# Performance work log

Measured on AMD Instinct MI355X. Metric: run time of the kernel, lower is better.

## Reference

```python
import jax, jax.numpy as jnp
import numpy as np

B, S, D, H, F, E, K = 2, 2048, 1024, 16, 4096, 8, 2
DH = D // H
EPS = 1e-6  # RMSNorm eps (torch nn.RMSNorm default ~ fp32 machine eps; 1e-6 used here)


def _rmsnorm(x, w):
    return x * jax.lax.rsqrt(jnp.mean(x * x, axis=-1, keepdims=True) + EPS) * w


def setup_inputs() -> dict:
    key = jax.random.key(0)
    ks = jax.random.split(key, 16)
    std = 0.02
    return {
        "x": jax.random.normal(ks[0], (B, S, D), jnp.float32),
        "norm1_w": jnp.ones((D,), jnp.float32),
        "norm2_w": jnp.ones((D,), jnp.float32),
        "w_qkv": jax.random.normal(ks[1], (D, 3 * D), jnp.float32) * std,
        "b_qkv": jnp.zeros((3 * D,), jnp.float32),
        "w_o": jax.random.normal(ks[2], (D, D), jnp.float32) * std,
        "b_o": jnp.zeros((D,), jnp.float32),
        "router_w": jax.random.normal(ks[3], (D, E), jnp.float32) * std,
        "router_b": jnp.zeros((E,), jnp.float32),
        "w1": jax.random.normal(ks[4], (E, D, F), jnp.float32) * std,
        "b1": jnp.zeros((E, F), jnp.float32),
        "w2": jax.random.normal(ks[5], (E, F, D), jnp.float32) * std,
        "b2": jnp.zeros((E, D), jnp.float32),
    }


def reference(x, norm1_w, norm2_w, w_qkv, b_qkv, w_o, b_o,
              router_w, router_b, w1, b1, w2, b2):
    # ---- pre-norm causal multi-head attention ----
    h = _rmsnorm(x, norm1_w)
    qkv = h @ w_qkv + b_qkv                                  # [B,S,3D]
    q, k, v = jnp.split(qkv, 3, axis=-1)
    q = q.reshape(B, S, H, DH).transpose(0, 2, 1, 3)         # [B,H,S,DH]
    k = k.reshape(B, S, H, DH).transpose(0, 2, 1, 3)
    v = v.reshape(B, S, H, DH).transpose(0, 2, 1, 3)
    scores = jnp.einsum('bhqd,bhkd->bhqk', q, k) / jnp.sqrt(jnp.asarray(DH, x.dtype))
    causal = jnp.tril(jnp.ones((S, S), bool))
    scores = jnp.where(causal, scores, jnp.asarray(-1e9, x.dtype))
    attn = jax.nn.softmax(scores, axis=-1)
    ao = jnp.einsum('bhqk,bhkd->bhqd', attn, v).transpose(0, 2, 1, 3).reshape(B, S, D)
    x = x + (ao @ w_o + b_o)

    # ---- pre-norm top-k MoE feed-forward ----
    h2 = _rmsnorm(x, norm2_w)
    t = h2.reshape(-1, D)                                    # [T,D], T=B*S
    logits = t @ router_w + router_b                         # [T,E]
    probs = jax.nn.softmax(logits, axis=-1)
    topv, topi = jax.lax.top_k(probs, K)                     # [T,K]
    gates_k = topv / jnp.sum(topv, axis=-1, keepdims=True)   # renormalized top-k gates
    oh = jax.nn.one_hot(topi, E, dtype=x.dtype)              # [T,K,E]
    gates = jnp.einsum('tke,tk->te', oh, gates_k)            # dense gates, zero off top-k

    out = jnp.zeros_like(t)
    for e in range(E):                                       # fixed small expert loop
        he = jax.nn.gelu(t @ w1[e] + b1[e], approximate=False)
        ye = he @ w2[e] + b2[e]
        out = out + gates[:, e:e + 1] * ye

    # load-balancing aux loss: E * sum_e f_e * P_e
    f = jnp.mean(jnp.sum(oh, axis=1), axis=0)                # fraction routed to each expert
    P = jnp.mean(probs, axis=0)                              # mean router prob per expert
    aux_loss = jnp.asarray(E, x.dtype) * jnp.sum(f * P)

    x = x + out.reshape(B, S, D)
    return (x, aux_loss)
```

## Files before the change

### kernel.cpp

```cpp
#include <hip/hip_runtime.h>
#include <math.h>

#define TB 2
#define TS 2048
#define TD 1024
#define TH 16
#define TDH 64
#define TF 4096
#define TE 8
#define TT 4096
#define PSTR (TB*TH*TS*TDH)

typedef __attribute__((ext_vector_type(8))) __bf16 bf16x8;
typedef __attribute__((ext_vector_type(4))) float f32x4;
typedef __attribute__((ext_vector_type(8))) short short8;
typedef __attribute__((ext_vector_type(4))) unsigned short ushort4v;
typedef __attribute__((ext_vector_type(4))) float fvec4;

__device__ inline unsigned short f2bf(float f) {
  union { float f; unsigned int u; } v; v.f = f;
  unsigned int u = v.u;
  unsigned int r = (u + 0x7FFFu + ((u >> 16) & 1u)) >> 16;
  return (unsigned short)r;
}
__device__ inline float bf2f(unsigned short h) {
  union { unsigned int u; float f; } v; v.u = ((unsigned int)h) << 16; return v.f;
}
__device__ inline void split2(float x, unsigned short& h, unsigned short& m) {
  h = f2bf(x);
  m = f2bf(x - bf2f(h));
}

__device__ inline f32x4 mfma_bf16(short8 a, short8 b, f32x4 c) {
  return __builtin_amdgcn_mfma_f32_16x16x32_bf16(
      __builtin_bit_cast(bf16x8, a), __builtin_bit_cast(bf16x8, b), c, 0, 0, 0);
}

__device__ inline void gload16(void* g, void* l) {
  __builtin_amdgcn_global_load_lds(
      (__attribute__((address_space(1))) void*)g,
      (__attribute__((address_space(3))) void*)l, 16, 0, 0);
}

__global__ __launch_bounds__(256)
void tcvt_kernel(const float* __restrict__ In, unsigned short* __restrict__ Out,
                 int R, int C) {
  __shared__ float tile[32][33];
  In  += (size_t)blockIdx.z * R * C;
  Out += (size_t)blockIdx.z * R * C;
  int c0 = blockIdx.x * 32, r0 = blockIdx.y * 32;
  int tx = threadIdx.x & 31, ty = threadIdx.x >> 5;
#pragma unroll
  for (int i = 0; i < 4; ++i)
    tile[ty + 8*i][tx] = In[(size_t)(r0 + ty + 8*i) * C + c0 + tx];
  __syncthreads();
#pragma unroll
  for (int i = 0; i < 4; ++i)
    Out[(size_t)(c0 + ty + 8*i) * R + r0 + tx] = f2bf(tile[tx][ty + 8*i]);
}

__global__ __launch_bounds__(256)
void tcvt_split_kernel(const float* __restrict__ In,
                       unsigned short* __restrict__ O0,
                       unsigned short* __restrict__ O1, int R, int C) {
  __shared__ float tile[32][33];
  int c0 = blockIdx.x * 32, r0 = blockIdx.y * 32;
  int tx = threadIdx.x & 31, ty = threadIdx.x >> 5;
#pragma unroll
  for (int i = 0; i < 4; ++i)
    tile[ty + 8*i][tx] = In[(size_t)(r0 + ty + 8*i) * C + c0 + tx];
  __syncthreads();
#pragma unroll
  for (int i = 0; i < 4; ++i) {
    float v = tile[tx][ty + 8*i];
    unsigned short h, m; split2(v, h, m);
    size_t idx = (size_t)(c0 + ty + 8*i) * R + r0 + tx;
    O0[idx] = h; O1[idx] = m;
  }
}

__global__ __launch_bounds__(256)
void rmsnorm_kernel(const float* __restrict__ X, const float* __restrict__ W,
                    unsigned short* __restrict__ O) {
  int row = blockIdx.x;
  int tid = threadIdx.x;
  int lane = tid & 63, wave = tid >> 6;
  const float* xr = X + (size_t)row * TD;
  fvec4 v = *(const fvec4*)(xr + tid * 4);
  float ss = v[0]*v[0] + v[1]*v[1] + v[2]*v[2] + v[3]*v[3];
#pragma unroll
  for (int msk = 1; msk < 64; msk <<= 1) ss += __shfl_xor(ss, msk);
  __shared__ float red[4];
  if (lane == 0) red[wave] = ss;
  __syncthreads();
  ss = red[0] + red[1] + red[2] + red[3];
  float rs = rsqrtf(ss * (1.0f / TD) + 1e-6f);
  fvec4 wv = *(const fvec4*)(W + tid * 4);
  ushort4v o;
#pragma unroll
  for (int j = 0; j < 4; ++j) o[j] = f2bf(v[j] * rs * wv[j]);
  *(ushort4v*)(O + (size_t)row * TD + tid * 4) = o;
}

__global__ __launch_bounds__(256)
void rmsnorm_split_kernel(const float* __restrict__ X, const float* __restrict__ W,
                          unsigned short* __restrict__ O0,
                          unsigned short* __restrict__ O1) {
  int row = blockIdx.x;
  int tid = threadIdx.x;
  int lane = tid & 63, wave = tid >> 6;
  const float* xr = X + (size_t)row * TD;
  fvec4 v = *(const fvec4*)(xr + tid * 4);
  float ss = v[0]*v[0] + v[1]*v[1] + v[2]*v[2] + v[3]*v[3];
#pragma unroll
  for (int msk = 1; msk < 64; msk <<= 1) ss += __shfl_xor(ss, msk);
  __shared__ float red[4];
  if (lane == 0) red[wave] = ss;
  __syncthreads();
  ss = red[0] + red[1] + red[2] + red[3];
  float rs = rsqrtf(ss * (1.0f / TD) + 1e-6f);
  fvec4 wv = *(const fvec4*)(W + tid * 4);
  ushort4v o0, o1;
#pragma unroll
  for (int j = 0; j < 4; ++j) {
    unsigned short h, m; split2(v[j] * rs * wv[j], h, m);
    o0[j] = h; o1[j] = m;
  }
  size_t idx = (size_t)row * TD + tid * 4;
  *(ushort4v*)(O0 + idx) = o0;
  *(ushort4v*)(O1 + idx) = o1;
}

template<int MODE>
__global__ __launch_bounds__(256)
void gemm2(const unsigned short* __restrict__ A0,
           const unsigned short* __restrict__ A1,
           const unsigned short* __restrict__ B0,
           const unsigned short* __restrict__ B1,
           const float* __restrict__ bias, int Kd,
           float* __restrict__ outF, const float* __restrict__ resid,
           unsigned short* __restrict__ S0,
           unsigned short* __restrict__ S1) {
  __shared__ __align__(16) char As0[8192], As1[8192];
  __shared__ __align__(16) char Bs0[8192], Bs1[8192];
  const int tid = threadIdx.x;
  const int lane = tid & 63;
  const int wave = tid >> 6;
  const int wr = wave >> 1, wc = wave & 1;
  const int g = lane >> 4;
  const int l15 = lane & 15;
  const int m0 = blockIdx.y * 128;
  const int n0 = blockIdx.x * 128;

  f32x4 acc[4][4] = {};

  for (int k0 = 0; k0 < Kd; k0 += 32) {
#pragma unroll
    for (int i = 0; i < 2; ++i) {
      int c = tid + i * 256;
      int lr = c >> 2;
      int c8 = (c & 3) * 8;
      int soff = (lr * 64 + c8 * 2) ^ ((lr & 3) << 4);
      size_t aoff = (size_t)(m0 + lr) * Kd + k0 + c8;
      *(short8*)(As0 + soff) = *(const short8*)(A0 + aoff);
      *(short8*)(As1 + soff) = *(const short8*)(A1 + aoff);
      size_t boff = (size_t)(n0 + lr) * Kd + k0 + c8;
      *(short8*)(Bs0 + soff) = *(const short8*)(B0 + boff);
      *(short8*)(Bs1 + soff) = *(const short8*)(B1 + boff);
    }
    __syncthreads();

    short8 a0f[4], a1f[4], b0f[4], b1f[4];
#pragma unroll
    for (int mi = 0; mi < 4; ++mi) {
      int row = wr * 64 + mi * 16 + l15;
      int off = (row * 64 + g * 16) ^ ((row & 3) << 4);
      a0f[mi] = *(const short8*)(As0 + off);
      a1f[mi] = *(const short8*)(As1 + off);
    }
#pragma unroll
    for (int ni = 0; ni < 4; ++ni) {
      int row = wc * 64 + ni * 16 + l15;
      int off = (row * 64 + g * 16) ^ ((row & 3) << 4);
      b0f[ni] = *(const short8*)(Bs0 + off);
      b1f[ni] = *(const short8*)(Bs1 + off);
    }
#pragma unroll
    for (int mi = 0; mi < 4; ++mi)
#pragma unroll
      for (int ni = 0; ni < 4; ++ni) {
        f32x4 t = acc[mi][ni];
        t = mfma_bf16(a0f[mi], b0f[ni], t);
        t = mfma_bf16(a0f[mi], b1f[ni], t);
        t = mfma_bf16(a1f[mi], b0f[ni], t);
        acc[mi][ni] = t;
      }
    __syncthreads();
  }

#pragma unroll
  for (int mi = 0; mi < 4; ++mi) {
#pragma unroll
    for (int ni = 0; ni < 4; ++ni) {
      int n = n0 + wc * 64 + ni * 16 + l15;
      float bv = bias[n];
      if (MODE == 0) {
        int part = n >> 10, d = n & 1023, hh = d >> 6, dh = d & 63;
        int s0r = m0 + wr * 64 + mi * 16 + g * 4;
        int b = s0r >> 11, s_ = s0r & 2047;
        int bh = b * TH + hh;
        if (part < 2) {
          size_t base = (size_t)part * PSTR + (size_t)bh * (TS * TDH) + (size_t)s_ * TDH + dh;
#pragma unroll
          for (int r = 0; r < 4; ++r) {
            unsigned short h, m; split2(acc[mi][ni][r] + bv, h, m);
            size_t idx = base + (size_t)r * TDH;
            S0[idx] = h; S1[idx] = m;
          }
        } else {
          ushort4v o0, o1;
#pragma unroll
          for (int r = 0; r < 4; ++r) {
            unsigned short h, m; split2(acc[mi][ni][r] + bv, h, m);
            o0[r] = h; o1[r] = m;
          }
          size_t idx = 2 * (size_t)PSTR + (size_t)bh * (TS * TDH) + (size_t)dh * TS + s_;
          *(ushort4v*)(S0 + idx) = o0;
          *(ushort4v*)(S1 + idx) = o1;
        }
      } else {
#pragma unroll
        for (int r = 0; r < 4; ++r) {
          int m = m0 + wr * 64 + mi * 16 + g * 4 + r;
          size_t idx = (size_t)m * TD + n;
          outF[idx] = acc[mi][ni][r] + bv + resid[idx];
        }
      }
    }
  }
}

__global__ __launch_bounds__(512, 4)
void attn2_kernel(const unsigned short* __restrict__ S0,
                  const unsigned short* __restrict__ S1,
                  unsigned short* __restrict__ A0,
                  unsigned short* __restrict__ A1) {
  __shared__ __align__(16) char Kt0[8192], Kt1[8192];
  __shared__ __align__(16) char Vt0[8192], Vt1[8192];
  __shared__ __align__(16) char Pt0[16384], Pt1[16384];

  const int tid = threadIdx.x;
  const int lane = tid & 63;
  const int wave = tid >> 6;
  const int g = lane >> 4, l15 = lane & 15;

  const int bh = blockIdx.y;
  const int b = bh >> 4, hh = bh & 15;

  const size_t qbase = (size_t)bh * TS * TDH;
  const size_t kbase = (size_t)PSTR + qbase;
  const size_t vbase = 2 * (size_t)PSTR + qbase;

  for (int half = 0; half < 2; ++half) {
    const int qtb = half ? (15 - (int)blockIdx.x) : (int)blockIdx.x;
    const int qlo = qtb * 128 + wave * 16;

    short8 aq0[2], aq1[2];
#pragma unroll
    for (int c = 0; c < 2; ++c) {
      size_t qo = qbase + (size_t)(qlo + l15) * TDH + c * 32 + g * 8;
      aq0[c] = *(const short8*)(S0 + qo);
      aq1[c] = *(const short8*)(S1 + qo);
    }

    f32x4 accv[4] = {};
    float m_[4] = {-1e30f, -1e30f, -1e30f, -1e30f};
    float l_[4] = {0.f, 0.f, 0.f, 0.f};

    const int ktmax = 2 * qtb + 1;
    for (int kt = 0; kt <= ktmax; ++kt) {
      __syncthreads();
      {
        int row = tid >> 3, ch = tid & 7;
        int off = (row * 128 + ch * 16) ^ ((row & 7) << 4);
        size_t kg = kbase + (size_t)(kt * 64 + row) * TDH + ch * 8;
        *(short8*)(Kt0 + off) = *(const short8*)(S0 + kg);
        *(short8*)(Kt1 + off) = *(const short8*)(S1 + kg);
        size_t vg = vbase + (size_t)row * TS + kt * 64 + ch * 8;
        *(short8*)(Vt0 + off) = *(const short8*)(S0 + vg);
        *(short8*)(Vt1 + off) = *(const short8*)(S1 + vg);
      }
      __syncthreads();

      if (kt * 64 > qlo + 15) continue;
      const bool needmask = (kt * 64 + 63 > qlo);

      f32x4 sf[4] = {};
#pragma unroll
      for (int kb = 0; kb < 4; ++kb) {
#pragma unroll
        for (int c = 0; c < 2; ++c) {
          int krow = kb * 16 + l15;
          int off = (krow * 128 + (c * 32 + g * 8) * 2) ^ ((krow & 7) << 4);
          short8 bk0 = *(const short8*)(Kt0 + off);
          short8 bk1 = *(const short8*)(Kt1 + off);
          f32x4 t = sf[kb];
          t = mfma_bf16(aq0[c], bk0, t);
          t = mfma_bf16(aq0[c], bk1, t);
          t = mfma_bf16(aq1[c], bk0, t);
          sf[kb] = t;
        }
      }

      float pv[4][4];
#pragma unroll
      for (int r = 0; r < 4; ++r) {
        float s0 = sf[0][r] * 0.125f, s1 = sf[1][r] * 0.125f;
        float s2 = sf[2][r] * 0.125f, s3 = sf[3][r] * 0.125f;
        if (needmask) {
          int qg = qlo + g * 4 + r;
          int k0g = kt * 64 + l15;
          if (k0g      > qg) s0 = -1e30f;
          if (k0g + 16 > qg) s1 = -1e30f;
          if (k0g + 32 > qg) s2 = -1e30f;
          if (k0g + 48 > qg) s3 = -1e30f;
        }
        float mx = fmaxf(fmaxf(s0, s1), fmaxf(s2, s3));
#pragma unroll
        for (int msk = 1; msk < 16; msk <<= 1) mx = fmaxf(mx, __shfl_xor(mx, msk));
        float nm = fmaxf(m_[r], mx);
        float sc = __expf(m_[r] - nm);
        float p0 = __expf(s0 - nm), p1 = __expf(s1 - nm);
        float p2 = __expf(s2 - nm), p3 = __expf(s3 - nm);
        float rs = p0 + p1 + p2 + p3;
#pragma unroll
        for (int msk = 1; msk < 16; msk <<= 1) rs += __shfl_xor(rs, msk);
        m_[r] = nm;
        l_[r] = l_[r] * sc + rs;
#pragma unroll
        for (int dhb = 0; dhb < 4; ++dhb) accv[dhb][r] *= sc;
        pv[0][r] = p0; pv[1][r] = p1; pv[2][r] = p2; pv[3][r] = p3;
      }

      char* P0 = Pt0 + wave * 2048;
      char* P1 = Pt1 + wave * 2048;
#pragma unroll
      for (int kb = 0; kb < 4; ++kb) {
#pragma unroll
        for (int r = 0; r < 4; ++r) {
          int prow = g * 4 + r;
          int key = kb * 16 + l15;
          int off = (prow * 128 + key * 2) ^ ((prow & 7) << 4);
          unsigned short h, m; split2(pv[kb][r], h, m);
          *(unsigned short*)(P0 + off) = h;
          *(unsigned short*)(P1 + off) = m;
        }
      }
      short8 pa0[2], pa1[2];
#pragma unroll
      for (int c = 0; c < 2; ++c) {
        int off = (l15 * 128 + (c * 32 + g * 8) * 2) ^ ((l15 & 7) << 4);
        pa0[c] = *(const short8*)(P0 + off);
        pa1[c] = *(const short8*)(P1 + off);
      }
#pragma unroll
      for (int dhb = 0; dhb < 4; ++dhb) {
#pragma unroll
        for (int c = 0; c < 2; ++c) {
          int dh = dhb * 16 + l15;
          int off = (dh * 128 + (c * 32 + g * 8) * 2) ^ ((dh & 7) << 4);
          short8 bv0 = *(const short8*)(Vt0 + off);
          short8 bv1 = *(const short8*)(Vt1 + off);
          f32x4 t = accv[dhb];
          t = mfma_bf16(pa0[c], bv0, t);
          t = mfma_bf16(pa0[c], bv1, t);
          t = mfma_bf16(pa1[c], bv0, t);
          accv[dhb] = t;
        }
      }
    }

#pragma unroll
    for (int dhb = 0; dhb < 4; ++dhb) {
#pragma unroll
      for (int r = 0; r < 4; ++r) {
        int srow = qlo + g * 4 + r;
        int col = hh * 64 + dhb * 16 + l15;
        unsigned short h, m; split2(accv[dhb][r] / l_[r], h, m);
        size_t idx = ((size_t)(b * TS + srow)) * TD + col;
        A0[idx] = h; A1[idx] = m;
      }
    }
  }
}

template<int MODE>
__global__ __launch_bounds__(256)
void gemm_bt(const unsigned short* __restrict__ A,
             const unsigned short* __restrict__ Bt,
             const float* __restrict__ bias,
             int N, int Kd,
             float* __restrict__ ysl,
             unsigned short* __restrict__ outH,
             const int* __restrict__ seg_off,
             const int* __restrict__ seg_cnt,
             const int* __restrict__ token_perm,
             const float* __restrict__ gate_perm) {
  __shared__ __align__(16) unsigned short As[4096];
  __shared__ __align__(16) unsigned short Bs[4096];
  __shared__ int tok[128];

  const int tid = threadIdx.x;
  const int lane = tid & 63;
  const int w = tid >> 6;
  const int wr = w >> 1, wc = w & 1;
  const int g = lane >> 4;
  const int l15 = lane & 15;

  const int e = blockIdx.z;
  const int m0 = blockIdx.y * 128;
  const int n0 = blockIdx.x * 128;
  const int off = seg_off[e];
  const int Mrows = seg_cnt[e];
  if (m0 >= Mrows) return;
  Bt += (size_t)e * N * Kd;
  bias += (size_t)e * N;
  if (tid < 128) {
    int r = m0 + tid;
    int rc = (r < Mrows) ? r : (Mrows - 1);
    tok[tid] = (MODE == 2) ? token_perm[off + rc] : (off + rc);
  }
  __syncthreads();

  const int c_swz = (lane & 3) ^ ((lane >> 2) & 3);
  const unsigned short* aptr[2];
  const unsigned short* bptr[2];
  unsigned short* AsB[2];
  unsigned short* BsB[2];
#pragma unroll
  for (int j = 0; j < 2; ++j) {
    int r = (w * 2 + j) * 16 + (lane >> 2);
    aptr[j] = A + (size_t)tok[r] * Kd + c_swz * 8;
    bptr[j] = Bt + (size_t)(n0 + r) * Kd + c_swz * 8;
    AsB[j] = &As[(w * 2 + j) * 512];
    BsB[j] = &Bs[(w * 2 + j) * 512];
  }

  f32x4 acc[4][4] = {};

  for (int k0 = 0; k0 < Kd; k0 += 32) {
#pragma unroll
    for (int j = 0; j < 2; ++j) {
      gload16((void*)(aptr[j] + k0), AsB[j]);
      gload16((void*)(bptr[j] + k0), BsB[j]);
    }
    __syncthreads();

    short8 af[4], bfr[4];
#pragma unroll
    for (int mi = 0; mi < 4; ++mi) {
      int row = wr * 64 + mi * 16 + l15;
      af[mi] = *(const short8*)((const char*)As + ((row * 64 + g * 16) ^ ((row & 3) << 4)));
    }
#pragma unroll
    for (int ni = 0; ni < 4; ++ni) {
      int row = wc * 64 + ni * 16 + l15;
      bfr[ni] = *(const short8*)((const char*)Bs + ((row * 64 + g * 16) ^ ((row & 3) << 4)));
    }
#pragma unroll
    for (int mi = 0; mi < 4; ++mi)
#pragma unroll
      for (int ni = 0; ni < 4; ++ni)
        acc[mi][ni] = mfma_bf16(af[mi], bfr[ni], acc[mi][ni]);
    __syncthreads();
  }

#pragma unroll
  for (int mi = 0; mi < 4; ++mi) {
#pragma unroll
    for (int ni = 0; ni < 4; ++ni) {
      int n = n0 + wc * 64 + ni * 16 + l15;
      float bv = bias[n];
#pragma unroll
      for (int r = 0; r < 4; ++r) {
        int mloc = m0 + wr * 64 + mi * 16 + g * 4 + r;
        if (mloc >= Mrows) continue;
        float val = acc[mi][ni][r] + bv;
        if (MODE == 2) {
          float ge = 0.5f * val * (1.0f + erff(val * 0.70710678118654752f));
          outH[(size_t)(off + mloc) * TF + n] = f2bf(ge);
        } else {
          float gv = gate_perm[off + mloc];
          ysl[(size_t)(off + mloc) * TD + n] = gv * val;
        }
      }
    }
  }
}

__global__ __launch_bounds__(256)
void moe_reduce_kernel(const float* __restrict__ ys, const int* __restrict__ tslot,
                       float* __restrict__ out) {
  int t = blockIdx.x;
  int d = threadIdx.x * 4;
  fvec4 a = *(const fvec4*)(ys + (size_t)tslot[t * 2] * TD + d);
  fvec4 b = *(const fvec4*)(ys + (size_t)tslot[t * 2 + 1] * TD + d);
  float* o = out + (size_t)t * TD + d;
  fvec4 c = *(const fvec4*)o;
#pragma unroll
  for (int j = 0; j < 4; ++j) c[j] += a[j] + b[j];
  *(fvec4*)o = c;
}

__global__ __launch_bounds__(256)
void router_kernel(const float* __restrict__ X1, const float* __restrict__ N2W,
                   const float* __restrict__ RW, const float* __restrict__ RB,
                   int* __restrict__ top_e, float* __restrict__ top_g,
                   int* __restrict__ counts, float* __restrict__ p_sum) {
  __shared__ float s_psum[TE];
  __shared__ int s_cnt[TE];
  if (threadIdx.x < TE) { s_psum[threadIdx.x] = 0.f; s_cnt[threadIdx.x] = 0; }
  __syncthreads();
  int lane = threadIdx.x & 63, wave = threadIdx.x >> 6;
  for (int it = 0; it < 16; ++it) {
    int t = (blockIdx.x * 4 + wave) * 16 + it;
    const float* xr = X1 + (size_t)t * TD;
    float vals[16]; float ss = 0.f;
#pragma unroll
    for (int i = 0; i < 16; ++i) { float xv = xr[i * 64 + lane]; vals[i] = xv; ss += xv * xv; }
#pragma unroll
    for (int msk = 1; msk < 64; msk <<= 1) ss += __shfl_xor(ss, msk);
    float rs = rsqrtf(ss * (1.0f / TD) + 1e-6f);
    float acc[TE] = {};
#pragma unroll
    for (int i = 0; i < 16; ++i) {
      int d = i * 64 + lane;
      float nv = vals[i] * rs * N2W[d];
      const float* rwp = RW + (size_t)d * TE;
#pragma unroll
      for (int e2 = 0; e2 < TE; ++e2) acc[e2] += nv * rwp[e2];
    }
#pragma unroll
    for (int msk = 1; msk < 64; msk <<= 1)
#pragma unroll
      for (int e2 = 0; e2 < TE; ++e2) acc[e2] += __shfl_xor(acc[e2], msk);
    if (lane == 0) {
      float lg[TE]; float mx = -1e30f;
      for (int e2 = 0; e2 < TE; ++e2) { lg[e2] = acc[e2] + RB[e2]; mx = fmaxf(mx, lg[e2]); }
      float sum = 0.f, pe[TE];
      for (int e2 = 0; e2 < TE; ++e2) { pe[e2] = expf(lg[e2] - mx); sum += pe[e2]; }
      float inv = 1.0f / sum;
      for (int e2 = 0; e2 < TE; ++e2) atomicAdd(&s_psum[e2], pe[e2] * inv);
      int i1 = 0;
      for (int e2 = 1; e2 < TE; ++e2) if (lg[e2] > lg[i1]) i1 = e2;
      int i2 = (i1 == 0) ? 1 : 0;
      for (int e2 = 0; e2 < TE; ++e2) if (e2 != i1 && lg[e2] > lg[i2]) i2 = e2;
      float g1 = pe[i1], g2 = pe[i2], gs = g1 + g2;
      top_e[t * 2] = i1; top_e[t * 2 + 1] = i2;
      top_g[t * 2] = g1 / gs; top_g[t * 2 + 1] = g2 / gs;
      atomicAdd(&s_cnt[i1], 1); atomicAdd(&s_cnt[i2], 1);
    }
  }
  __syncthreads();
  if (threadIdx.x < TE) {
    atomicAdd(&p_sum[threadIdx.x], s_psum[threadIdx.x]);
    atomicAdd(&counts[threadIdx.x], s_cnt[threadIdx.x]);
  }
}

__global__ void zero_meta_kernel(int* counts, float* p_sum) {
  int t = threadIdx.x;
  if (t < TE) { counts[t] = 0; p_sum[t] = 0.f; }
}

__global__ void offsets_kernel(const int* counts, int* offs, int* cursor) {
  if (threadIdx.x == 0) {
    int o = 0;
    for (int e2 = 0; e2 < TE; ++e2) { offs[e2] = o; o += counts[e2]; }
  }
  if (threadIdx.x < TE) cursor[threadIdx.x] = 0;
}

__global__ __launch_bounds__(256)
void fill_kernel(const int* __restrict__ top_e, const float* __restrict__ top_g,
                 const int* __restrict__ offs, int* __restrict__ cursor,
                 int* __restrict__ token_perm, float* __restrict__ gate_perm,
                 int* __restrict__ tslot) {
  __shared__ int s_cnt[TE], s_base[TE];
  if (threadIdx.x < TE) s_cnt[threadIdx.x] = 0;
  __syncthreads();
  int t = blockIdx.x * 256 + threadIdx.x;
  int e0 = top_e[t * 2], e1 = top_e[t * 2 + 1];
  int r0 = atomicAdd(&s_cnt[e0], 1);
  int r1 = atomicAdd(&s_cnt[e1], 1);
  __syncthreads();
  if (threadIdx.x < TE)
    s_base[threadIdx.x] = atomicAdd(&cursor[threadIdx.x], s_cnt[threadIdx.x]);
  __syncthreads();
  int p0 = offs[e0] + s_base[e0] + r0;
  int p1 = offs[e1] + s_base[e1] + r1;
  token_perm[p0] = t; gate_perm[p0] = top_g[t * 2];
  token_perm[p1] = t; gate_perm[p1] = top_g[t * 2 + 1];
  tslot[t * 2] = p0; tslot[t * 2 + 1] = p1;
}

__global__ void aux_kernel(const int* counts, const float* p_sum, float* outv) {
  if (threadIdx.x == 0) {
    float a = 0.f;
    for (int e2 = 0; e2 < TE; ++e2)
      a += ((float)counts[e2] / (float)TT) * (p_sum[e2] / (float)TT);
    outv[0] = (float)TE * a;
  }
}

extern "C" void kernel_launch(void* const* d_in, const int* in_sizes, int n_in,
                              void* d_out, int out_size, void* d_ws, size_t ws_size,
                              hipStream_t stream) {
  const float* x     = (const float*)d_in[0];
  const float* n1w   = (const float*)d_in[1];
  const float* n2w   = (const float*)d_in[2];
  const float* w_qkv = (const float*)d_in[3];
  const float* b_qkv = (const float*)d_in[4];
  const float* w_o   = (const float*)d_in[5];
  const float* b_o   = (const float*)d_in[6];
  const float* rw    = (const float*)d_in[7];
  const float* rb    = (const float*)d_in[8];
  const float* w1    = (const float*)d_in[9];
  const float* b1    = (const float*)d_in[10];
  const float* w2    = (const float*)d_in[11];
  const float* b2    = (const float*)d_in[12];
  float* out = (float*)d_out;
  char* ws = (char*)d_ws;

  size_t o = 0;
  auto give = [&](size_t bytes) -> char* {
    char* p = ws + o;
    o += (bytes + 255) & ~(size_t)255;
    return p;
  };
  unsigned short* w1T = (unsigned short*)give(8ull * 4096 * 1024 * 2);
  unsigned short* w2T = (unsigned short*)give(8ull * 1024 * 4096 * 2);
  unsigned short* wo0 = (unsigned short*)give(1024ull * 1024 * 2);
  unsigned short* wo1 = (unsigned short*)give(1024ull * 1024 * 2);
  unsigned short* h2  = (unsigned short*)give((size_t)TT * TD * 2);
  int*   counts = (int*)give(TE * 4);
  int*   cursor = (int*)give(TE * 4);
  int*   offs   = (int*)give(TE * 4);
  float* psum   = (float*)give(TE * 4);
  int*   top_e  = (int*)give(2ull * TT * 4);
  float* top_g  = (float*)give(2ull * TT * 4);
  int*   tperm  = (int*)give(2ull * TT * 4);
  float* gperm  = (float*)give(2ull * TT * 4);
  int*   tslot  = (int*)give(2ull * TT * 4);
  unsigned short* wq0 = (unsigned short*)give(3072ull * 1024 * 2);
  unsigned short* wq1 = (unsigned short*)give(3072ull * 1024 * 2);
  float* ys = (float*)give(2ull * TT * TD * 4);
  char* poolB = give(2ull * TT * TD * 2);
  unsigned short* h10 = (unsigned short*)poolB;
  unsigned short* h11 = (unsigned short*)(poolB + (size_t)TT * TD * 2);
  unsigned short* ao0 = h10; unsigned short* ao1 = h11;
  char* poolC = give(64ull * 1024 * 1024);
  unsigned short* qs0 = (unsigned short*)poolC;
  unsigned short* qs1 = (unsigned short*)(poolC + 3ull * PSTR * 2);
  unsigned short* he  = (unsigned short*)poolC;

  tcvt_split_kernel<<<dim3(96, 32, 1), 256, 0, stream>>>(w_qkv, wq0, wq1, 1024, 3072);
  tcvt_split_kernel<<<dim3(32, 32, 1), 256, 0, stream>>>(w_o, wo0, wo1, 1024, 1024);
  tcvt_kernel<<<dim3(128, 32, 8), 256, 0, stream>>>(w1, w1T, 1024, 4096);
  tcvt_kernel<<<dim3(32, 128, 8), 256, 0, stream>>>(w2, w2T, 4096, 1024);

  rmsnorm_split_kernel<<<dim3(TT), 256, 0, stream>>>(x, n1w, h10, h11);
  gemm2<0><<<dim3(24, 32, 1), 256, 0, stream>>>(
      h10, h11, wq0, wq1, b_qkv, 1024, nullptr, nullptr, qs0, qs1);
  attn2_kernel<<<dim3(8, 32, 1), 512, 0, stream>>>(qs0, qs1, ao0, ao1);
  gemm2<1><<<dim3(8, 32, 1), 256, 0, stream>>>(
      ao0, ao1, wo0, wo1, b_o, 1024, out, x, nullptr, nullptr);

  rmsnorm_kernel<<<dim3(TT), 256, 0, stream>>>(out, n2w, h2);
  zero_meta_kernel<<<dim3(1), 64, 0, stream>>>(counts, psum);
  router_kernel<<<dim3(64), 256, 0, stream>>>(out, n2w, rw, rb, top_e, top_g, counts, psum);
  offsets_kernel<<<dim3(1), 64, 0, stream>>>(counts, offs, cursor);
  fill_kernel<<<dim3(TT / 256), 256, 0, stream>>>(top_e, top_g, offs, cursor, tperm, gperm, tslot);
  gemm_bt<2><<<dim3(32, 32, 8), 256, 0, stream>>>(
      h2, w1T, b1, 4096, 1024, nullptr, he, offs, counts, tperm, gperm);
  gemm_bt<3><<<dim3(8, 32, 8), 256, 0, stream>>>(
      he, w2T, b2, 1024, 4096, ys, nullptr, offs, counts, tperm, gperm);
  moe_reduce_kernel<<<dim3(TT), 256, 0, stream>>>(ys, tslot, out);
  aux_kernel<<<dim3(1), 64, 0, stream>>>(counts, psum, out + (size_t)TT * TD);
}
```

Baseline: 786.8 us.

## Double-buffer GEMM LDS tiles with async global_load_lds prefetch in both GEMMs

Converts gemm2 (the split-bf16 three-MFMA GEMM) from register-staged global-to-LDS copies to direct global_load_lds, and double-buffers LDS in both gemm2 and the MoE gemm_bt. The next K-tile is prefetched while the current one is computed, using s_waitcnt vmcnt and raw s_barrier in place of __syncthreads. The XOR swizzle pattern changes to match the new lane-to-row mapping of the async loads. This doubles LDS use, which can lower occupancy, and relies on hand-counted vmcnt values being correct.

```diff
diff --git a/kernel.cpp b/kernel.cpp
--- a/kernel.cpp
+++ b/kernel.cpp
@@ -36,9 +36,9 @@
       __builtin_bit_cast(bf16x8, a), __builtin_bit_cast(bf16x8, b), c, 0, 0, 0);
 }
 
-__device__ inline void gload16(void* g, void* l) {
+__device__ inline void gload16(const void* g, void* l) {
   __builtin_amdgcn_global_load_lds(
-      (__attribute__((address_space(1))) void*)g,
+      (const __attribute__((address_space(1))) void*)g,
       (__attribute__((address_space(3))) void*)l, 16, 0, 0);
 }
 
@@ -141,62 +141,84 @@
            float* __restrict__ outF, const float* __restrict__ resid,
            unsigned short* __restrict__ S0,
            unsigned short* __restrict__ S1) {
-  __shared__ __align__(16) char As0[8192], As1[8192];
-  __shared__ __align__(16) char Bs0[8192], Bs1[8192];
+  __shared__ __align__(16) unsigned short As0[2][4096], As1[2][4096];
+  __shared__ __align__(16) unsigned short Bs0[2][4096], Bs1[2][4096];
   const int tid = threadIdx.x;
   const int lane = tid & 63;
-  const int wave = tid >> 6;
-  const int wr = wave >> 1, wc = wave & 1;
+  const int w = tid >> 6;
+  const int wr = w >> 1, wc = w & 1;
   const int g = lane >> 4;
   const int l15 = lane & 15;
   const int m0 = blockIdx.y * 128;
   const int n0 = blockIdx.x * 128;
 
+  const int c_swz = (lane & 3) ^ ((lane >> 3) & 3);
+  const unsigned short *a0p[2], *a1p[2], *b0p[2], *b1p[2];
+  int ldsrow[2];
+#pragma unroll
+  for (int j = 0; j < 2; ++j) {
+    int r16 = w * 2 + j;
+    int r = r16 * 16 + (lane >> 2);
+    a0p[j] = A0 + (size_t)(m0 + r) * Kd + c_swz * 8;
+    a1p[j] = A1 + (size_t)(m0 + r) * Kd + c_swz * 8;
+    b0p[j] = B0 + (size_t)(n0 + r) * Kd + c_swz * 8;
+    b1p[j] = B1 + (size_t)(n0 + r) * Kd + c_swz * 8;
+    ldsrow[j] = r16 * 512;
+  }
+
+#define G2_STAGE(p, koff)                              \
+  {                                                    \
+    _Pragma("unroll")                                  \
+    for (int j = 0; j < 2; ++j) {                      \
+      gload16(a0p[j] + (koff), &As0[p][ldsrow[j]]);    \
+      gload16(a1p[j] + (koff), &As1[p][ldsrow[j]]);    \
+      gload16(b0p[j] + (koff), &Bs0[p][ldsrow[j]]);    \
+      gload16(b1p[j] + (koff), &Bs1[p][ldsrow[j]]);    \
+    }                                                  \
+  }
+
   f32x4 acc[4][4] = {};
-
-  for (int k0 = 0; k0 < Kd; k0 += 32) {
-#pragma unroll
-    for (int i = 0; i < 2; ++i) {
-      int c = tid + i * 256;
-      int lr = c >> 2;
-      int c8 = (c & 3) * 8;
-      int soff = (lr * 64 + c8 * 2) ^ ((lr & 3) << 4);
-      size_t aoff = (size_t)(m0 + lr) * Kd + k0 + c8;
-      *(short8*)(As0 + soff) = *(const short8*)(A0 + aoff);
-      *(short8*)(As1 + soff) = *(const short8*)(A1 + aoff);
-      size_t boff = (size_t)(n0 + lr) * Kd + k0 + c8;
-      *(short8*)(Bs0 + soff) = *(const short8*)(B0 + boff);
-      *(short8*)(Bs1 + soff) = *(const short8*)(B1 + boff);
-    }
-    __syncthreads();
+  const int nt = Kd >> 5;
+
+  G2_STAGE(0, 0);
+  for (int t = 0; t < nt; ++t) {
+    const int p = t & 1;
+    if (t + 1 < nt) {
+      G2_STAGE(p ^ 1, (t + 1) * 32);
+      asm volatile("s_waitcnt vmcnt(8)" ::: "memory");
+    } else {
+      asm volatile("s_waitcnt vmcnt(0)" ::: "memory");
+    }
+    __builtin_amdgcn_s_barrier();
 
     short8 a0f[4], a1f[4], b0f[4], b1f[4];
 #pragma unroll
     for (int mi = 0; mi < 4; ++mi) {
       int row = wr * 64 + mi * 16 + l15;
-      int off = (row * 64 + g * 16) ^ ((row & 3) << 4);
-      a0f[mi] = *(const short8*)(As0 + off);
-      a1f[mi] = *(const short8*)(As1 + off);
+      int off = (row * 64 + g * 16) ^ (((row >> 1) & 3) << 4);
+      a0f[mi] = *(const short8*)((const char*)As0[p] + off);
+      a1f[mi] = *(const short8*)((const char*)As1[p] + off);
     }
 #pragma unroll
     for (int ni = 0; ni < 4; ++ni) {
       int row = wc * 64 + ni * 16 + l15;
-      int off = (row * 64 + g * 16) ^ ((row & 3) << 4);
-      b0f[ni] = *(const short8*)(Bs0 + off);
-      b1f[ni] = *(const short8*)(Bs1 + off);
+      int off = (row * 64 + g * 16) ^ (((row >> 1) & 3) << 4);
+      b0f[ni] = *(const short8*)((const char*)Bs0[p] + off);
+      b1f[ni] = *(const short8*)((const char*)Bs1[p] + off);
     }
 #pragma unroll
     for (int mi = 0; mi < 4; ++mi)
 #pragma unroll
       for (int ni = 0; ni < 4; ++ni) {
-        f32x4 t = acc[mi][ni];
-        t = mfma_bf16(a0f[mi], b0f[ni], t);
-        t = mfma_bf16(a0f[mi], b1f[ni], t);
-        t = mfma_bf16(a1f[mi], b0f[ni], t);
-        acc[mi][ni] = t;
-      }
-    __syncthreads();
-  }
+        f32x4 tacc = acc[mi][ni];
+        tacc = mfma_bf16(a0f[mi], b0f[ni], tacc);
+        tacc = mfma_bf16(a0f[mi], b1f[ni], tacc);
+        tacc = mfma_bf16(a1f[mi], b0f[ni], tacc);
+        acc[mi][ni] = tacc;
+      }
+    __builtin_amdgcn_s_barrier();
+  }
+#undef G2_STAGE
 
 #pragma unroll
   for (int mi = 0; mi < 4; ++mi) {
@@ -406,8 +428,8 @@
              const int* __restrict__ seg_cnt,
              const int* __restrict__ token_perm,
              const float* __restrict__ gate_perm) {
-  __shared__ __align__(16) unsigned short As[4096];
-  __shared__ __align__(16) unsigned short Bs[4096];
+  __shared__ __align__(16) unsigned short As[2][4096];
+  __shared__ __align__(16) unsigned short Bs[2][4096];
   __shared__ int tok[128];
 
   const int tid = threadIdx.x;
@@ -432,48 +454,63 @@
   }
   __syncthreads();
 
-  const int c_swz = (lane & 3) ^ ((lane >> 2) & 3);
+  const int c_swz = (lane & 3) ^ ((lane >> 3) & 3);
   const unsigned short* aptr[2];
   const unsigned short* bptr[2];
-  unsigned short* AsB[2];
-  unsigned short* BsB[2];
+  int ldsrow[2];
 #pragma unroll
   for (int j = 0; j < 2; ++j) {
-    int r = (w * 2 + j) * 16 + (lane >> 2);
+    int r16 = w * 2 + j;
+    int r = r16 * 16 + (lane >> 2);
     aptr[j] = A + (size_t)tok[r] * Kd + c_swz * 8;
     bptr[j] = Bt + (size_t)(n0 + r) * Kd + c_swz * 8;
-    AsB[j] = &As[(w * 2 + j) * 512];
-    BsB[j] = &Bs[(w * 2 + j) * 512];
+    ldsrow[j] = r16 * 512;
+  }
+
+#define GB_STAGE(p, koff)                           \
+  {                                                 \
+    _Pragma("unroll")                               \
+    for (int j = 0; j < 2; ++j) {                   \
+      gload16(aptr[j] + (koff), &As[p][ldsrow[j]]); \
+      gload16(bptr[j] + (koff), &Bs[p][ldsrow[j]]); \
+    }                                               \
   }
 
   f32x4 acc[4][4] = {};
-
-  for (int k0 = 0; k0 < Kd; k0 += 32) {
-#pragma unroll
-    for (int j = 0; j < 2; ++j) {
-      gload16((void*)(aptr[j] + k0), AsB[j]);
-      gload16((void*)(bptr[j] + k0), BsB[j]);
-    }
-    __syncthreads();
+  const int nt = Kd >> 5;
+
+  GB_STAGE(0, 0);
+  for (int t = 0; t < nt; ++t) {
+    const int p = t & 1;
+    if (t + 1 < nt) {
+      GB_STAGE(p ^ 1, (t + 1) * 32);
+      asm volatile("s_waitcnt vmcnt(4)" ::: "memory");
+    } else {
+      asm volatile("s_waitcnt vmcnt(0)" ::: "memory");
+    }
+    __builtin_amdgcn_s_barrier();
 
     short8 af[4], bfr[4];
 #pragma unroll
     for (int mi = 0; mi < 4; ++mi) {
       int row = wr * 64 + mi * 16 + l15;
-      af[mi] = *(const short8*)((const char*)As + ((row * 64 + g * 16) ^ ((row & 3) << 4)));
+      int o2 = (row * 64 + g * 16) ^ (((row >> 1) & 3) << 4);
+      af[mi] = *(const short8*)((const char*)As[p] + o2);
     }
 #pragma unroll
     for (int ni = 0; ni < 4; ++ni) {
       int row = wc * 64 + ni * 16 + l15;
-      bfr[ni] = *(const short8*)((const char*)Bs + ((row * 64 + g * 16) ^ ((row & 3) << 4)));
+      int o2 = (row * 64 + g * 16) ^ (((row >> 1) & 3) << 4);
+      bfr[ni] = *(const short8*)((const char*)Bs[p] + o2);
     }
 #pragma unroll
     for (int mi = 0; mi < 4; ++mi)
 #pragma unroll
       for (int ni = 0; ni < 4; ++ni)
         acc[mi][ni] = mfma_bf16(af[mi], bfr[ni], acc[mi][ni]);
-    __syncthreads();
-  }
+    __builtin_amdgcn_s_barrier();
+  }
+#undef GB_STAGE
 
 #pragma unroll
   for (int mi = 0; mi < 4; ++mi) {
```

Result: faster. 749.4 us (-4.8%).
